# Kernel tuning notes

Hardware: AMD Instinct MI355X
Metric: run time of the kernel (lower is better)

The kernel has to match this reference:

```python
import jax, jax.numpy as jnp
import numpy as np

N, P, C = 100000, 64, 128
DIST_TH = 0.1


def setup_inputs() -> dict:
    key = jax.random.key(0)
    ks = jax.random.split(key, 12)
    xyz = jax.random.uniform(ks[0], (N, 3), jnp.float32) * 10.0  # room coords in [0,10)^3
    feature = jax.random.normal(ks[1], (N, C), jnp.float32)
    center = jax.random.uniform(ks[2], (P, 3), jnp.float32) * 10.0
    normal = jax.random.normal(ks[3], (P, 3), jnp.float32)
    normal = normal / jnp.linalg.norm(normal, axis=1, keepdims=True)
    pmin = center - 1.5  # axis-aligned extent used on axes 0,1
    pmax = center + 1.5
    inp = {
        'feature': feature, 'xyz': xyz,
        'plane_center': center, 'plane_normal': normal,
        'plane_min': pmin, 'plane_max': pmax,
        'W1': jax.random.normal(ks[4], (C, 2 * C), jnp.float32) * (1.0 / np.sqrt(C)),
        's1': jnp.ones((2 * C,), jnp.float32), 'b1': jnp.zeros((2 * C,), jnp.float32),
        'W2': jax.random.normal(ks[5], (2 * C, C), jnp.float32) * (1.0 / np.sqrt(2 * C)),
        's2': jnp.ones((C,), jnp.float32), 'b2': jnp.zeros((C,), jnp.float32),
        'W3': jax.random.normal(ks[6], (C, 1), jnp.float32) * (1.0 / np.sqrt(C)),
        'b3': jnp.zeros((1,), jnp.float32),
        'Wa': jax.random.normal(ks[7], (C, C), jnp.float32) * (1.0 / np.sqrt(C)),
        'Wm': jax.random.normal(ks[8], (C, C), jnp.float32) * (1.0 / np.sqrt(C)),
        'bm': jnp.zeros((C,), jnp.float32),
    }
    return inp


def reference(feature, xyz, plane_center, plane_normal, plane_min, plane_max,
              W1, s1, b1, W2, s2, b2, W3, b3, Wa, Wm, bm):
    # pointwise MLP (shared across planes): fc1 (conv+BN+ReLU), fc2 (conv+BN+ReLU)
    h = jax.nn.relu((feature @ W1) * s1 + b1)          # [N, 2C]
    h2 = jax.nn.relu((h @ W2) * s2 + b2)               # [N, C] == plane_feature
    logit = (h2 @ W3 + b3)[:, 0]                        # [N] fc3 logits (plane_result)

    # per-plane point membership masks (dense [N, P])
    proj = xyz @ plane_normal.T                         # [N, P]
    offs = jnp.sum(plane_center * plane_normal, axis=1) # [P]
    dist_mask = jnp.abs(proj - offs[None, :]) < DIST_TH
    rng = ((xyz[:, None, 0] >= plane_min[None, :, 0]) & (xyz[:, None, 0] < plane_max[None, :, 0]) &
           (xyz[:, None, 1] >= plane_min[None, :, 1]) & (xyz[:, None, 1] < plane_max[None, :, 1]))
    mask = dist_mask & rng                              # [N, P]

    on_sel = jax.nn.sigmoid(logit) > 0.5                # [N]
    on_mask = (mask & on_sel[:, None]).astype(feature.dtype)
    off_mask = (mask & ~on_sel[:, None]).astype(feature.dtype)

    # attention pooling: masked softmax over points, per plane, per channel
    a = h2 @ Wa                                         # [N, C] att activations
    e = jnp.exp(a - jnp.max(a, axis=0, keepdims=True))  # stable exp, [N, C]
    eh = e * h2

    def att_pool(m):                                    # m: [N, P] float
        num = jnp.einsum('np,nc->pc', m, eh)
        den = jnp.einsum('np,nc->pc', m, e)
        agg = num / (den + 1e-9)                        # masked-softmax weighted sum
        return jax.nn.relu(agg @ Wm + bm)               # att_pooling.mlp (conv+ReLU)

    ori = jnp.concatenate([plane_center, plane_normal, plane_min, plane_max], axis=1)  # [P, 12]
    on_feat = jnp.concatenate([att_pool(on_mask), ori], axis=1)    # [P, C+12]
    off_feat = jnp.concatenate([att_pool(off_mask), ori], axis=1)  # [P, C+12]
    return logit, on_feat, off_feat
```

## Files before the change

kernel.cpp:

```cpp
#include <hip/hip_runtime.h>

#define NPTS 100000
#define P 64
#define C 128
#define CHUNKS 16
#define CHUNK_PTS 6250
#define CHUNK_PAD 6400

typedef __bf16 bf16_t;
typedef __bf16 bf16x4 __attribute__((ext_vector_type(4)));
typedef __bf16 bf16x8 __attribute__((ext_vector_type(8)));
typedef float floatx4 __attribute__((ext_vector_type(4)));


__global__ __launch_bounds__(256) void prep_kernel(
    const float* __restrict__ W1, const float* __restrict__ s1,
    const float* __restrict__ W2, const float* __restrict__ s2,
    const float* __restrict__ Wa,
    bf16_t* __restrict__ W1t, bf16_t* __restrict__ W2t, bf16_t* __restrict__ Wat)
{
  int i0 = blockIdx.x * blockDim.x + threadIdx.x;
  int stride = gridDim.x * blockDim.x;
  for (int i = i0; i < 256 * 128; i += stride) {
    int n = i >> 7, k = i & 127;
    W1t[i] = (bf16_t)(W1[k * 256 + n] * s1[n]);
  }
  for (int i = i0; i < 128 * 256; i += stride) {
    int n = i >> 8, k = i & 255;
    W2t[i] = (bf16_t)(W2[k * 128 + n] * s2[n]);
  }
  for (int i = i0; i < 128 * 128; i += stride) {
    int n = i >> 7, k = i & 127;
    Wat[i] = (bf16_t)(Wa[k * 128 + n]);
  }
}

__device__ __forceinline__ void process_tile(
    bf16_t* A1, bf16_t* Hs, bf16_t* aB,
    const float* w3S, const float* b1S, const float* b2S, float b3v,
    const bf16_t* __restrict__ W1t, const bf16_t* __restrict__ W2t,
    const bf16_t* __restrict__ Wat,
    bf16_t* __restrict__ rec, float* __restrict__ out_logit,
    int m0, int tid, int wave, int lane, int quad, int l16)
{
  const floatx4 zero4 = {0.f, 0.f, 0.f, 0.f};

  {
    floatx4 acc[4][4];
#pragma unroll
    for (int mt = 0; mt < 4; ++mt)
#pragma unroll
      for (int nt = 0; nt < 4; ++nt) acc[mt][nt] = zero4;
#pragma unroll
    for (int kt = 0; kt < 4; ++kt) {
      bf16x8 af[4], bf[4];
#pragma unroll
      for (int mt = 0; mt < 4; ++mt)
        af[mt] = *(const bf16x8*)(A1 + (mt * 16 + l16) * 136 + kt * 32 + quad * 8);
#pragma unroll
      for (int nt = 0; nt < 4; ++nt)
        bf[nt] = *(const bf16x8*)(W1t + (wave * 64 + nt * 16 + l16) * 128 + kt * 32 + quad * 8);
#pragma unroll
      for (int mt = 0; mt < 4; ++mt)
#pragma unroll
        for (int nt = 0; nt < 4; ++nt)
          acc[mt][nt] = __builtin_amdgcn_mfma_f32_16x16x32_bf16(af[mt], bf[nt], acc[mt][nt], 0, 0, 0);
    }
#pragma unroll
    for (int nt = 0; nt < 4; ++nt) {
      int col = wave * 64 + nt * 16 + l16;
      float bias = b1S[col];
#pragma unroll
      for (int mt = 0; mt < 4; ++mt)
#pragma unroll
        for (int r = 0; r < 4; ++r) {
          float hv = fmaxf(acc[mt][nt][r] + bias, 0.f);
          Hs[(mt * 16 + quad * 4 + r) * 264 + col] = (bf16_t)hv;
        }
    }
  }
  __syncthreads();

  {
    floatx4 acc[4][2];
#pragma unroll
    for (int mt = 0; mt < 4; ++mt) { acc[mt][0] = zero4; acc[mt][1] = zero4; }
#pragma unroll
    for (int kt = 0; kt < 8; ++kt) {
      bf16x8 af[4], bf[2];
#pragma unroll
      for (int mt = 0; mt < 4; ++mt)
        af[mt] = *(const bf16x8*)(Hs + (mt * 16 + l16) * 264 + kt * 32 + quad * 8);
#pragma unroll
      for (int nt = 0; nt < 2; ++nt)
        bf[nt] = *(const bf16x8*)(W2t + (wave * 32 + nt * 16 + l16) * 256 + kt * 32 + quad * 8);
#pragma unroll
      for (int mt = 0; mt < 4; ++mt)
#pragma unroll
        for (int nt = 0; nt < 2; ++nt)
          acc[mt][nt] = __builtin_amdgcn_mfma_f32_16x16x32_bf16(af[mt], bf[nt], acc[mt][nt], 0, 0, 0);
    }
#pragma unroll
    for (int nt = 0; nt < 2; ++nt) {
      int col = wave * 32 + nt * 16 + l16;
      float bias = b2S[col];
#pragma unroll
      for (int mt = 0; mt < 4; ++mt)
#pragma unroll
        for (int r = 0; r < 4; ++r) {
          float hv = fmaxf(acc[mt][nt][r] + bias, 0.f);
          A1[(mt * 16 + quad * 4 + r) * 136 + col] = (bf16_t)hv;
        }
    }
  }
  __syncthreads();

  {
    floatx4 acc[4][2];
#pragma unroll
    for (int mt = 0; mt < 4; ++mt) { acc[mt][0] = zero4; acc[mt][1] = zero4; }
#pragma unroll
    for (int kt = 0; kt < 4; ++kt) {
      bf16x8 af[4], bf[2];
#pragma unroll
      for (int mt = 0; mt < 4; ++mt)
        af[mt] = *(const bf16x8*)(A1 + (mt * 16 + l16) * 136 + kt * 32 + quad * 8);
#pragma unroll
      for (int nt = 0; nt < 2; ++nt)
        bf[nt] = *(const bf16x8*)(Wat + (wave * 32 + nt * 16 + l16) * 128 + kt * 32 + quad * 8);
#pragma unroll
      for (int mt = 0; mt < 4; ++mt)
#pragma unroll
        for (int nt = 0; nt < 2; ++nt)
          acc[mt][nt] = __builtin_amdgcn_mfma_f32_16x16x32_bf16(af[mt], bf[nt], acc[mt][nt], 0, 0, 0);
    }
#pragma unroll
    for (int nt = 0; nt < 2; ++nt) {
      int col = wave * 32 + nt * 16 + l16;
#pragma unroll
      for (int mt = 0; mt < 4; ++mt)
#pragma unroll
        for (int r = 0; r < 4; ++r)
          aB[(mt * 16 + quad * 4 + r) * 136 + col] = (bf16_t)acc[mt][nt][r];
    }
  }
  __syncthreads();

  {
    const int m = tid >> 2, g = tid & 3, c0g = g * 32;
    const int mg = m0 + m;
    float lsum = 0.f;
#pragma unroll
    for (int cc = 0; cc < 4; ++cc) {
      bf16x8 v = *(const bf16x8*)(A1 + m * 136 + c0g + cc * 8);
#pragma unroll
      for (int j = 0; j < 8; ++j)
        lsum += (float)v[j] * w3S[c0g + cc * 8 + j];
    }
    lsum += __shfl_xor(lsum, 1);
    lsum += __shfl_xor(lsum, 2);
    if (mg < NPTS && g == 0) out_logit[mg] = lsum + b3v;
  }

  for (int i = tid; i < 64 * 64; i += 256) {
    int pt = i >> 6, slot = i & 63;
    if (m0 + pt < NPTS) {
      const bf16_t* src = (slot < 32) ? (aB + pt * 136 + slot * 4)
                                      : (A1 + pt * 136 + (slot - 32) * 4);
      uint2 v = *(const uint2*)src;
      *(uint2*)(rec + (size_t)(m0 + pt) * 256 + slot * 4) = v;
    }
  }
}

__global__ __launch_bounds__(256) void main_kernel(
    const float* __restrict__ feature,
    const float* __restrict__ b1, const float* __restrict__ b2,
    const float* __restrict__ W3, const float* __restrict__ b3,
    const bf16_t* __restrict__ W1t, const bf16_t* __restrict__ W2t,
    const bf16_t* __restrict__ Wat,
    bf16_t* __restrict__ rec, float* __restrict__ out_logit)
{
  __shared__ __align__(16) char smem[17408 + 33792 + 512 + 1024 + 512];
  bf16_t* A1  = (bf16_t*)smem;
  bf16_t* Hs  = (bf16_t*)(smem + 17408);
  bf16_t* aB  = (bf16_t*)(smem + 17408);
  float*  w3S = (float*)(smem + 17408 + 33792);
  float*  b1S = (float*)(smem + 17408 + 33792 + 512);
  float*  b2S = (float*)(smem + 17408 + 33792 + 512 + 1024);

  const int tid  = threadIdx.x;
  const int wave = tid >> 6, lane = tid & 63;
  const int quad = lane >> 4, l16 = lane & 15;
  const int m0 = blockIdx.x * 128;

  if (tid < 128) w3S[tid] = W3[tid];
  if (tid < 128) b2S[tid] = b2[tid];
  b1S[tid] = b1[tid];
  const float b3v = b3[0];

  const int r0 = tid >> 5, c4 = tid & 31;

#pragma unroll
  for (int j = 0; j < 8; ++j) {
    int r = r0 + j * 8;
    float4 v = make_float4(0.f, 0.f, 0.f, 0.f);
    if (m0 + r < NPTS) v = *(const float4*)(feature + (size_t)(m0 + r) * C + c4 * 4);
    bf16x4 o = {(bf16_t)v.x, (bf16_t)v.y, (bf16_t)v.z, (bf16_t)v.w};
    *(bf16x4*)(A1 + r * 136 + c4 * 4) = o;
  }
  __syncthreads();

  float4 f2[8];
#pragma unroll
  for (int j = 0; j < 8; ++j) {
    int r = r0 + j * 8;
    f2[j] = make_float4(0.f, 0.f, 0.f, 0.f);
    if (m0 + 64 + r < NPTS)
      f2[j] = *(const float4*)(feature + (size_t)(m0 + 64 + r) * C + c4 * 4);
  }

  process_tile(A1, Hs, aB, w3S, b1S, b2S, b3v, W1t, W2t, Wat, rec, out_logit,
               m0, tid, wave, lane, quad, l16);
  __syncthreads();

#pragma unroll
  for (int j = 0; j < 8; ++j) {
    int r = r0 + j * 8;
    bf16x4 o = {(bf16_t)f2[j].x, (bf16_t)f2[j].y, (bf16_t)f2[j].z, (bf16_t)f2[j].w};
    *(bf16x4*)(A1 + r * 136 + c4 * 4) = o;
  }
  __syncthreads();

  process_tile(A1, Hs, aB, w3S, b1S, b2S, b3v, W1t, W2t, Wat, rec, out_logit,
               m0 + 64, tid, wave, lane, quad, l16);
}

__global__ __launch_bounds__(256) void pool_kernel(
    const float* __restrict__ xyz, const float* __restrict__ out_logit,
    const bf16_t* __restrict__ rec,
    const float* __restrict__ ctr, const float* __restrict__ nrm,
    const float* __restrict__ pmn, const float* __restrict__ pmx,
    float* __restrict__ partial)
{
  const int plane = blockIdx.x >> 4;
  const int chunk = blockIdx.x & 15;
  const int tid = threadIdx.x, lane = tid & 63;

  __shared__ float accS[4][128];
  for (int i = tid; i < 512; i += 256) ((float*)accS)[i] = 0.f;

  const float nx = nrm[plane * 3], ny = nrm[plane * 3 + 1], nz = nrm[plane * 3 + 2];
  const float offs = ctr[plane * 3] * nx + ctr[plane * 3 + 1] * ny + ctr[plane * 3 + 2] * nz;
  const float mnx = pmn[plane * 3], mny = pmn[plane * 3 + 1];
  const float mxx = pmx[plane * 3], mxy = pmx[plane * 3 + 1];
  __syncthreads();

  const int base = chunk * CHUNK_PTS;
  float nOn0 = 0, nOn1 = 0, dOn0 = 0, dOn1 = 0;
  float nOf0 = 0, nOf1 = 0, dOf0 = 0, dOf1 = 0;

  for (int i = tid; i < CHUNK_PAD; i += 256) {
    int pt = base + i;
    bool hit = false;
    if (i < CHUNK_PTS) {
      float x = xyz[pt * 3], y = xyz[pt * 3 + 1], z = xyz[pt * 3 + 2];
      float proj = x * nx + y * ny + z * nz;
      hit = (fabsf(proj - offs) < 0.1f) &&
            (x >= mnx) && (x < mxx) && (y >= mny) && (y < mxy);
    }
    unsigned long long m = __ballot(hit);
    while (m) {
      int l = __builtin_ctzll(m);
      m &= m - 1;
      int hpt = __shfl(pt, l);
      float lg = out_logit[hpt];
      const unsigned* r32 = (const unsigned*)(rec + (size_t)hpt * 256);
      unsigned ap = r32[lane];
      unsigned hp = r32[64 + lane];
      float a0 = __uint_as_float(ap << 16);
      float a1 = __uint_as_float(ap & 0xffff0000u);
      float h0 = __uint_as_float(hp << 16);
      float h1 = __uint_as_float(hp & 0xffff0000u);
      float e0 = __expf(a0), e1 = __expf(a1);
      if (lg > 0.f) { nOn0 += e0 * h0; nOn1 += e1 * h1; dOn0 += e0; dOn1 += e1; }
      else          { nOf0 += e0 * h0; nOf1 += e1 * h1; dOf0 += e0; dOf1 += e1; }
    }
  }

  atomicAdd(&accS[0][lane * 2],     nOn0);
  atomicAdd(&accS[0][lane * 2 + 1], nOn1);
  atomicAdd(&accS[1][lane * 2],     dOn0);
  atomicAdd(&accS[1][lane * 2 + 1], dOn1);
  atomicAdd(&accS[2][lane * 2],     nOf0);
  atomicAdd(&accS[2][lane * 2 + 1], nOf1);
  atomicAdd(&accS[3][lane * 2],     dOf0);
  atomicAdd(&accS[3][lane * 2 + 1], dOf1);
  __syncthreads();

  float* dst = partial + (size_t)blockIdx.x * 512;
  for (int i = tid; i < 512; i += 256) dst[i] = ((float*)accS)[i];
}

__global__ __launch_bounds__(256) void finalize_kernel(
    const float* __restrict__ partial,
    const float* __restrict__ Wm, const float* __restrict__ bm,
    const float* __restrict__ ctr, const float* __restrict__ nrm,
    const float* __restrict__ pmn, const float* __restrict__ pmx,
    float* __restrict__ out)
{
  int sel = blockIdx.x >> 6, p = blockIdx.x & 63;
  int tid = threadIdx.x, j = tid & 127, half = tid >> 7;
  __shared__ float numS[2][128], denS[2][128], aggS[128], sumS[2][128];

  const float* bp = partial + ((size_t)p * 16 + half * 8) * 512 + sel * 256;
  float num = 0.f, den = 0.f;
#pragma unroll
  for (int k = 0; k < 8; ++k) {
    num += bp[k * 512 + j];
    den += bp[k * 512 + 128 + j];
  }
  numS[half][j] = num;
  denS[half][j] = den;
  __syncthreads();
  if (tid < 128)
    aggS[tid] = (numS[0][tid] + numS[1][tid]) / (denS[0][tid] + denS[1][tid] + 1e-9f);
  __syncthreads();

  float s = 0.f;
  const int cbase = half * 64;
#pragma unroll 8
  for (int c = 0; c < 64; ++c)
    s += aggS[cbase + c] * Wm[(cbase + c) * C + j];
  sumS[half][j] = s;
  __syncthreads();

  float* dst = out + NPTS + sel * (P * 140) + p * 140;
  if (tid < 128)
    dst[tid] = fmaxf(sumS[0][tid] + sumS[1][tid] + bm[tid], 0.f);
  if (tid < 12) {
    float v;
    if (tid < 3)      v = ctr[p * 3 + tid];
    else if (tid < 6) v = nrm[p * 3 + tid - 3];
    else if (tid < 9) v = pmn[p * 3 + tid - 6];
    else              v = pmx[p * 3 + tid - 9];
    dst[C + tid] = v;
  }
}

extern "C" void kernel_launch(void* const* d_in, const int* in_sizes, int n_in,
                              void* d_out, int out_size, void* d_ws, size_t ws_size,
                              hipStream_t stream)
{
  const float* feature = (const float*)d_in[0];
  const float* xyz     = (const float*)d_in[1];
  const float* ctr     = (const float*)d_in[2];
  const float* nrm     = (const float*)d_in[3];
  const float* pmn     = (const float*)d_in[4];
  const float* pmx     = (const float*)d_in[5];
  const float* W1      = (const float*)d_in[6];
  const float* s1      = (const float*)d_in[7];
  const float* b1      = (const float*)d_in[8];
  const float* W2      = (const float*)d_in[9];
  const float* s2      = (const float*)d_in[10];
  const float* b2      = (const float*)d_in[11];
  const float* W3      = (const float*)d_in[12];
  const float* b3      = (const float*)d_in[13];
  const float* Wa      = (const float*)d_in[14];
  const float* Wm      = (const float*)d_in[15];
  const float* bm      = (const float*)d_in[16];
  float* out = (float*)d_out;

  char* ws = (char*)d_ws;
  bf16_t* W1t = (bf16_t*)(ws);
  bf16_t* W2t = (bf16_t*)(ws + 65536);
  bf16_t* Wat = (bf16_t*)(ws + 131072);
  bf16_t* rec = (bf16_t*)(ws + 163840);
  float* partial = (float*)(ws + 163840 + (size_t)NPTS * 512);

  prep_kernel<<<64, 256, 0, stream>>>(W1, s1, W2, s2, Wa, W1t, W2t, Wat);
  main_kernel<<<(NPTS + 127) / 128, 256, 0, stream>>>(
      feature, b1, b2, W3, b3, W1t, W2t, Wat, rec, out);
  pool_kernel<<<64 * CHUNKS, 256, 0, stream>>>(
      xyz, out, rec, ctr, nrm, pmn, pmx, partial);
  finalize_kernel<<<128, 256, 0, stream>>>(partial, Wm, bm, ctr, nrm, pmn, pmx, out);
}
```

Before: 196.9 us.

## Shrink MLP kernel tile to 32 points per block for higher occupancy

```diff
diff --git a/kernel.cpp b/kernel.cpp
--- a/kernel.cpp
+++ b/kernel.cpp
@@ -35,145 +35,7 @@
   }
 }
 
-__device__ __forceinline__ void process_tile(
-    bf16_t* A1, bf16_t* Hs, bf16_t* aB,
-    const float* w3S, const float* b1S, const float* b2S, float b3v,
-    const bf16_t* __restrict__ W1t, const bf16_t* __restrict__ W2t,
-    const bf16_t* __restrict__ Wat,
-    bf16_t* __restrict__ rec, float* __restrict__ out_logit,
-    int m0, int tid, int wave, int lane, int quad, int l16)
-{
-  const floatx4 zero4 = {0.f, 0.f, 0.f, 0.f};
-
-  {
-    floatx4 acc[4][4];
-#pragma unroll
-    for (int mt = 0; mt < 4; ++mt)
-#pragma unroll
-      for (int nt = 0; nt < 4; ++nt) acc[mt][nt] = zero4;
-#pragma unroll
-    for (int kt = 0; kt < 4; ++kt) {
-      bf16x8 af[4], bf[4];
-#pragma unroll
-      for (int mt = 0; mt < 4; ++mt)
-        af[mt] = *(const bf16x8*)(A1 + (mt * 16 + l16) * 136 + kt * 32 + quad * 8);
-#pragma unroll
-      for (int nt = 0; nt < 4; ++nt)
-        bf[nt] = *(const bf16x8*)(W1t + (wave * 64 + nt * 16 + l16) * 128 + kt * 32 + quad * 8);
-#pragma unroll
-      for (int mt = 0; mt < 4; ++mt)
-#pragma unroll
-        for (int nt = 0; nt < 4; ++nt)
-          acc[mt][nt] = __builtin_amdgcn_mfma_f32_16x16x32_bf16(af[mt], bf[nt], acc[mt][nt], 0, 0, 0);
-    }
-#pragma unroll
-    for (int nt = 0; nt < 4; ++nt) {
-      int col = wave * 64 + nt * 16 + l16;
-      float bias = b1S[col];
-#pragma unroll
-      for (int mt = 0; mt < 4; ++mt)
-#pragma unroll
-        for (int r = 0; r < 4; ++r) {
-          float hv = fmaxf(acc[mt][nt][r] + bias, 0.f);
-          Hs[(mt * 16 + quad * 4 + r) * 264 + col] = (bf16_t)hv;
-        }
-    }
-  }
-  __syncthreads();
-
-  {
-    floatx4 acc[4][2];
-#pragma unroll
-    for (int mt = 0; mt < 4; ++mt) { acc[mt][0] = zero4; acc[mt][1] = zero4; }
-#pragma unroll
-    for (int kt = 0; kt < 8; ++kt) {
-      bf16x8 af[4], bf[2];
-#pragma unroll
-      for (int mt = 0; mt < 4; ++mt)
-        af[mt] = *(const bf16x8*)(Hs + (mt * 16 + l16) * 264 + kt * 32 + quad * 8);
-#pragma unroll
-      for (int nt = 0; nt < 2; ++nt)
-        bf[nt] = *(const bf16x8*)(W2t + (wave * 32 + nt * 16 + l16) * 256 + kt * 32 + quad * 8);
-#pragma unroll
-      for (int mt = 0; mt < 4; ++mt)
-#pragma unroll
-        for (int nt = 0; nt < 2; ++nt)
-          acc[mt][nt] = __builtin_amdgcn_mfma_f32_16x16x32_bf16(af[mt], bf[nt], acc[mt][nt], 0, 0, 0);
-    }
-#pragma unroll
-    for (int nt = 0; nt < 2; ++nt) {
-      int col = wave * 32 + nt * 16 + l16;
-      float bias = b2S[col];
-#pragma unroll
-      for (int mt = 0; mt < 4; ++mt)
-#pragma unroll
-        for (int r = 0; r < 4; ++r) {
-          float hv = fmaxf(acc[mt][nt][r] + bias, 0.f);
-          A1[(mt * 16 + quad * 4 + r) * 136 + col] = (bf16_t)hv;
-        }
-    }
-  }
-  __syncthreads();
-
-  {
-    floatx4 acc[4][2];
-#pragma unroll
-    for (int mt = 0; mt < 4; ++mt) { acc[mt][0] = zero4; acc[mt][1] = zero4; }
-#pragma unroll
-    for (int kt = 0; kt < 4; ++kt) {
-      bf16x8 af[4], bf[2];
-#pragma unroll
-      for (int mt = 0; mt < 4; ++mt)
-        af[mt] = *(const bf16x8*)(A1 + (mt * 16 + l16) * 136 + kt * 32 + quad * 8);
-#pragma unroll
-      for (int nt = 0; nt < 2; ++nt)
-        bf[nt] = *(const bf16x8*)(Wat + (wave * 32 + nt * 16 + l16) * 128 + kt * 32 + quad * 8);
-#pragma unroll
-      for (int mt = 0; mt < 4; ++mt)
-#pragma unroll
-        for (int nt = 0; nt < 2; ++nt)
-          acc[mt][nt] = __builtin_amdgcn_mfma_f32_16x16x32_bf16(af[mt], bf[nt], acc[mt][nt], 0, 0, 0);
-    }
-#pragma unroll
-    for (int nt = 0; nt < 2; ++nt) {
-      int col = wave * 32 + nt * 16 + l16;
-#pragma unroll
-      for (int mt = 0; mt < 4; ++mt)
-#pragma unroll
-        for (int r = 0; r < 4; ++r)
-          aB[(mt * 16 + quad * 4 + r) * 136 + col] = (bf16_t)acc[mt][nt][r];
-    }
-  }
-  __syncthreads();
-
-  {
-    const int m = tid >> 2, g = tid & 3, c0g = g * 32;
-    const int mg = m0 + m;
-    float lsum = 0.f;
-#pragma unroll
-    for (int cc = 0; cc < 4; ++cc) {
-      bf16x8 v = *(const bf16x8*)(A1 + m * 136 + c0g + cc * 8);
-#pragma unroll
-      for (int j = 0; j < 8; ++j)
-        lsum += (float)v[j] * w3S[c0g + cc * 8 + j];
-    }
-    lsum += __shfl_xor(lsum, 1);
-    lsum += __shfl_xor(lsum, 2);
-    if (mg < NPTS && g == 0) out_logit[mg] = lsum + b3v;
-  }
-
-  for (int i = tid; i < 64 * 64; i += 256) {
-    int pt = i >> 6, slot = i & 63;
-    if (m0 + pt < NPTS) {
-      const bf16_t* src = (slot < 32) ? (aB + pt * 136 + slot * 4)
-                                      : (A1 + pt * 136 + (slot - 32) * 4);
-      uint2 v = *(const uint2*)src;
-      *(uint2*)(rec + (size_t)(m0 + pt) * 256 + slot * 4) = v;
-    }
-  }
-}
-
-__global__ __launch_bounds__(256) void main_kernel(
+__global__ __launch_bounds__(256, 6) void main_kernel(
     const float* __restrict__ feature,
     const float* __restrict__ b1, const float* __restrict__ b2,
     const float* __restrict__ W3, const float* __restrict__ b3,
@@ -181,59 +43,156 @@
     const bf16_t* __restrict__ Wat,
     bf16_t* __restrict__ rec, float* __restrict__ out_logit)
 {
-  __shared__ __align__(16) char smem[17408 + 33792 + 512 + 1024 + 512];
+  __shared__ __align__(16) char smem[8704 + 16896 + 512];
   bf16_t* A1  = (bf16_t*)smem;
-  bf16_t* Hs  = (bf16_t*)(smem + 17408);
-  bf16_t* aB  = (bf16_t*)(smem + 17408);
-  float*  w3S = (float*)(smem + 17408 + 33792);
-  float*  b1S = (float*)(smem + 17408 + 33792 + 512);
-  float*  b2S = (float*)(smem + 17408 + 33792 + 512 + 1024);
+  bf16_t* Hs  = (bf16_t*)(smem + 8704);
+  bf16_t* aB  = (bf16_t*)(smem + 8704);
+  float*  w3S = (float*)(smem + 8704 + 16896);
 
   const int tid  = threadIdx.x;
   const int wave = tid >> 6, lane = tid & 63;
   const int quad = lane >> 4, l16 = lane & 15;
-  const int m0 = blockIdx.x * 128;
+  const int m0 = blockIdx.x * 32;
 
   if (tid < 128) w3S[tid] = W3[tid];
-  if (tid < 128) b2S[tid] = b2[tid];
-  b1S[tid] = b1[tid];
-  const float b3v = b3[0];
-
-  const int r0 = tid >> 5, c4 = tid & 31;
-
-#pragma unroll
-  for (int j = 0; j < 8; ++j) {
-    int r = r0 + j * 8;
-    float4 v = make_float4(0.f, 0.f, 0.f, 0.f);
-    if (m0 + r < NPTS) v = *(const float4*)(feature + (size_t)(m0 + r) * C + c4 * 4);
+
+#pragma unroll
+  for (int j = 0; j < 4; ++j) {
+    int idx = j * 256 + tid;
+    int r = idx >> 5, c4 = idx & 31;
+    float4 v = *(const float4*)(feature + (size_t)(m0 + r) * C + c4 * 4);
     bf16x4 o = {(bf16_t)v.x, (bf16_t)v.y, (bf16_t)v.z, (bf16_t)v.w};
     *(bf16x4*)(A1 + r * 136 + c4 * 4) = o;
   }
   __syncthreads();
 
-  float4 f2[8];
-#pragma unroll
-  for (int j = 0; j < 8; ++j) {
-    int r = r0 + j * 8;
-    f2[j] = make_float4(0.f, 0.f, 0.f, 0.f);
-    if (m0 + 64 + r < NPTS)
-      f2[j] = *(const float4*)(feature + (size_t)(m0 + 64 + r) * C + c4 * 4);
-  }
-
-  process_tile(A1, Hs, aB, w3S, b1S, b2S, b3v, W1t, W2t, Wat, rec, out_logit,
-               m0, tid, wave, lane, quad, l16);
-  __syncthreads();
-
-#pragma unroll
-  for (int j = 0; j < 8; ++j) {
-    int r = r0 + j * 8;
-    bf16x4 o = {(bf16_t)f2[j].x, (bf16_t)f2[j].y, (bf16_t)f2[j].z, (bf16_t)f2[j].w};
-    *(bf16x4*)(A1 + r * 136 + c4 * 4) = o;
-  }
-  __syncthreads();
-
-  process_tile(A1, Hs, aB, w3S, b1S, b2S, b3v, W1t, W2t, Wat, rec, out_logit,
-               m0 + 64, tid, wave, lane, quad, l16);
+  const floatx4 zero4 = {0.f, 0.f, 0.f, 0.f};
+
+  {
+    floatx4 acc[2][4];
+#pragma unroll
+    for (int mt = 0; mt < 2; ++mt)
+#pragma unroll
+      for (int nt = 0; nt < 4; ++nt) acc[mt][nt] = zero4;
+#pragma unroll
+    for (int kt = 0; kt < 4; ++kt) {
+      bf16x8 af[2], bf[4];
+#pragma unroll
+      for (int mt = 0; mt < 2; ++mt)
+        af[mt] = *(const bf16x8*)(A1 + (mt * 16 + l16) * 136 + kt * 32 + quad * 8);
+#pragma unroll
+      for (int nt = 0; nt < 4; ++nt)
+        bf[nt] = *(const bf16x8*)(W1t + (wave * 64 + nt * 16 + l16) * 128 + kt * 32 + quad * 8);
+#pragma unroll
+      for (int mt = 0; mt < 2; ++mt)
+#pragma unroll
+        for (int nt = 0; nt < 4; ++nt)
+          acc[mt][nt] = __builtin_amdgcn_mfma_f32_16x16x32_bf16(af[mt], bf[nt], acc[mt][nt], 0, 0, 0);
+    }
+#pragma unroll
+    for (int nt = 0; nt < 4; ++nt) {
+      int col = wave * 64 + nt * 16 + l16;
+      float bias = b1[col];
+#pragma unroll
+      for (int mt = 0; mt < 2; ++mt)
+#pragma unroll
+        for (int r = 0; r < 4; ++r) {
+          float hv = fmaxf(acc[mt][nt][r] + bias, 0.f);
+          Hs[(mt * 16 + quad * 4 + r) * 264 + col] = (bf16_t)hv;
+        }
+    }
+  }
+  __syncthreads();
+
+  {
+    floatx4 acc[2][2];
+#pragma unroll
+    for (int mt = 0; mt < 2; ++mt) { acc[mt][0] = zero4; acc[mt][1] = zero4; }
+#pragma unroll
+    for (int kt = 0; kt < 8; ++kt) {
+      bf16x8 af[2], bf[2];
+#pragma unroll
+      for (int mt = 0; mt < 2; ++mt)
+        af[mt] = *(const bf16x8*)(Hs + (mt * 16 + l16) * 264 + kt * 32 + quad * 8);
+#pragma unroll
+      for (int nt = 0; nt < 2; ++nt)
+        bf[nt] = *(const bf16x8*)(W2t + (wave * 32 + nt * 16 + l16) * 256 + kt * 32 + quad * 8);
+#pragma unroll
+      for (int mt = 0; mt < 2; ++mt)
+#pragma unroll
+        for (int nt = 0; nt < 2; ++nt)
+          acc[mt][nt] = __builtin_amdgcn_mfma_f32_16x16x32_bf16(af[mt], bf[nt], acc[mt][nt], 0, 0, 0);
+    }
+#pragma unroll
+    for (int nt = 0; nt < 2; ++nt) {
+      int col = wave * 32 + nt * 16 + l16;
+      float bias = b2[col];
+#pragma unroll
+      for (int mt = 0; mt < 2; ++mt)
+#pragma unroll
+        for (int r = 0; r < 4; ++r) {
+          float hv = fmaxf(acc[mt][nt][r] + bias, 0.f);
+          A1[(mt * 16 + quad * 4 + r) * 136 + col] = (bf16_t)hv;
+        }
+    }
+  }
+  __syncthreads();
+
+  {
+    floatx4 acc[2][2];
+#pragma unroll
+    for (int mt = 0; mt < 2; ++mt) { acc[mt][0] = zero4; acc[mt][1] = zero4; }
+#pragma unroll
+    for (int kt = 0; kt < 4; ++kt) {
+      bf16x8 af[2], bf[2];
+#pragma unroll
+      for (int mt = 0; mt < 2; ++mt)
+        af[mt] = *(const bf16x8*)(A1 + (mt * 16 + l16) * 136 + kt * 32 + quad * 8);
+#pragma unroll
+      for (int nt = 0; nt < 2; ++nt)
+        bf[nt] = *(const bf16x8*)(Wat + (wave * 32 + nt * 16 + l16) * 128 + kt * 32 + quad * 8);
+#pragma unroll
+      for (int mt = 0; mt < 2; ++mt)
+#pragma unroll
+        for (int nt = 0; nt < 2; ++nt)
+          acc[mt][nt] = __builtin_amdgcn_mfma_f32_16x16x32_bf16(af[mt], bf[nt], acc[mt][nt], 0, 0, 0);
+    }
+#pragma unroll
+    for (int nt = 0; nt < 2; ++nt) {
+      int col = wave * 32 + nt * 16 + l16;
+#pragma unroll
+      for (int mt = 0; mt < 2; ++mt)
+#pragma unroll
+        for (int r = 0; r < 4; ++r)
+          aB[(mt * 16 + quad * 4 + r) * 136 + col] = (bf16_t)acc[mt][nt][r];
+    }
+  }
+  __syncthreads();
+
+  {
+    const int m = tid >> 3, g = tid & 7, c0g = g * 16;
+    float lsum = 0.f;
+#pragma unroll
+    for (int cc = 0; cc < 2; ++cc) {
+      bf16x8 v = *(const bf16x8*)(A1 + m * 136 + c0g + cc * 8);
+#pragma unroll
+      for (int j = 0; j < 8; ++j)
+        lsum += (float)v[j] * w3S[c0g + cc * 8 + j];
+    }
+    lsum += __shfl_xor(lsum, 1);
+    lsum += __shfl_xor(lsum, 2);
+    lsum += __shfl_xor(lsum, 4);
+    if (g == 0) out_logit[m0 + m] = lsum + b3[0];
+  }
+
+#pragma unroll
+  for (int i = tid; i < 32 * 64; i += 256) {
+    int pt = i >> 6, slot = i & 63;
+    const bf16_t* src = (slot < 32) ? (aB + pt * 136 + slot * 4)
+                                    : (A1 + pt * 136 + (slot - 32) * 4);
+    uint2 v = *(const uint2*)src;
+    *(uint2*)(rec + (size_t)(m0 + pt) * 256 + slot * 4) = v;
+  }
 }
 
 __global__ __launch_bounds__(256) void pool_kernel(
@@ -379,7 +338,7 @@
   float* partial = (float*)(ws + 163840 + (size_t)NPTS * 512);
 
   prep_kernel<<<64, 256, 0, stream>>>(W1, s1, W2, s2, Wa, W1t, W2t, Wat);
-  main_kernel<<<(NPTS + 127) / 128, 256, 0, stream>>>(
+  main_kernel<<<NPTS / 32, 256, 0, stream>>>(
       feature, b1, b2, W3, b3, W1t, W2t, Wat, rec, out);
   pool_kernel<<<64 * CHUNKS, 256, 0, stream>>>(
       xyz, out, rec, ctr, nrm, pmn, pmx, partial);
```

Result: slower. 204.1 us (+3.6%).

## Hold MLP weight fragments in registers and process one 64-point tile per block

Applied to the files above, without the earlier changes.

```diff
diff --git a/kernel.cpp b/kernel.cpp
--- a/kernel.cpp
+++ b/kernel.cpp
@@ -7,6 +7,9 @@
 #define CHUNK_PTS 6250
 #define CHUNK_PAD 6400
 
+#define SA 138
+#define SH 266
+
 typedef __bf16 bf16_t;
 typedef __bf16 bf16x4 __attribute__((ext_vector_type(4)));
 typedef __bf16 bf16x8 __attribute__((ext_vector_type(8)));
@@ -35,145 +38,7 @@
   }
 }
 
-__device__ __forceinline__ void process_tile(
-    bf16_t* A1, bf16_t* Hs, bf16_t* aB,
-    const float* w3S, const float* b1S, const float* b2S, float b3v,
-    const bf16_t* __restrict__ W1t, const bf16_t* __restrict__ W2t,
-    const bf16_t* __restrict__ Wat,
-    bf16_t* __restrict__ rec, float* __restrict__ out_logit,
-    int m0, int tid, int wave, int lane, int quad, int l16)
-{
-  const floatx4 zero4 = {0.f, 0.f, 0.f, 0.f};
-
-  {
-    floatx4 acc[4][4];
-#pragma unroll
-    for (int mt = 0; mt < 4; ++mt)
-#pragma unroll
-      for (int nt = 0; nt < 4; ++nt) acc[mt][nt] = zero4;
-#pragma unroll
-    for (int kt = 0; kt < 4; ++kt) {
-      bf16x8 af[4], bf[4];
-#pragma unroll
-      for (int mt = 0; mt < 4; ++mt)
-        af[mt] = *(const bf16x8*)(A1 + (mt * 16 + l16) * 136 + kt * 32 + quad * 8);
-#pragma unroll
-      for (int nt = 0; nt < 4; ++nt)
-        bf[nt] = *(const bf16x8*)(W1t + (wave * 64 + nt * 16 + l16) * 128 + kt * 32 + quad * 8);
-#pragma unroll
-      for (int mt = 0; mt < 4; ++mt)
-#pragma unroll
-        for (int nt = 0; nt < 4; ++nt)
-          acc[mt][nt] = __builtin_amdgcn_mfma_f32_16x16x32_bf16(af[mt], bf[nt], acc[mt][nt], 0, 0, 0);
-    }
-#pragma unroll
-    for (int nt = 0; nt < 4; ++nt) {
-      int col = wave * 64 + nt * 16 + l16;
-      float bias = b1S[col];
-#pragma unroll
-      for (int mt = 0; mt < 4; ++mt)
-#pragma unroll
-        for (int r = 0; r < 4; ++r) {
-          float hv = fmaxf(acc[mt][nt][r] + bias, 0.f);
-          Hs[(mt * 16 + quad * 4 + r) * 264 + col] = (bf16_t)hv;
-        }
-    }
-  }
-  __syncthreads();
-
-  {
-    floatx4 acc[4][2];
-#pragma unroll
-    for (int mt = 0; mt < 4; ++mt) { acc[mt][0] = zero4; acc[mt][1] = zero4; }
-#pragma unroll
-    for (int kt = 0; kt < 8; ++kt) {
-      bf16x8 af[4], bf[2];
-#pragma unroll
-      for (int mt = 0; mt < 4; ++mt)
-        af[mt] = *(const bf16x8*)(Hs + (mt * 16 + l16) * 264 + kt * 32 + quad * 8);
-#pragma unroll
-      for (int nt = 0; nt < 2; ++nt)
-        bf[nt] = *(const bf16x8*)(W2t + (wave * 32 + nt * 16 + l16) * 256 + kt * 32 + quad * 8);
-#pragma unroll
-      for (int mt = 0; mt < 4; ++mt)
-#pragma unroll
-        for (int nt = 0; nt < 2; ++nt)
-          acc[mt][nt] = __builtin_amdgcn_mfma_f32_16x16x32_bf16(af[mt], bf[nt], acc[mt][nt], 0, 0, 0);
-    }
-#pragma unroll
-    for (int nt = 0; nt < 2; ++nt) {
-      int col = wave * 32 + nt * 16 + l16;
-      float bias = b2S[col];
-#pragma unroll
-      for (int mt = 0; mt < 4; ++mt)
-#pragma unroll
-        for (int r = 0; r < 4; ++r) {
-          float hv = fmaxf(acc[mt][nt][r] + bias, 0.f);
-          A1[(mt * 16 + quad * 4 + r) * 136 + col] = (bf16_t)hv;
-        }
-    }
-  }
-  __syncthreads();
-
-  {
-    floatx4 acc[4][2];
-#pragma unroll
-    for (int mt = 0; mt < 4; ++mt) { acc[mt][0] = zero4; acc[mt][1] = zero4; }
-#pragma unroll
-    for (int kt = 0; kt < 4; ++kt) {
-      bf16x8 af[4], bf[2];
-#pragma unroll
-      for (int mt = 0; mt < 4; ++mt)
-        af[mt] = *(const bf16x8*)(A1 + (mt * 16 + l16) * 136 + kt * 32 + quad * 8);
-#pragma unroll
-      for (int nt = 0; nt < 2; ++nt)
-        bf[nt] = *(const bf16x8*)(Wat + (wave * 32 + nt * 16 + l16) * 128 + kt * 32 + quad * 8);
-#pragma unroll
-      for (int mt = 0; mt < 4; ++mt)
-#pragma unroll
-        for (int nt = 0; nt < 2; ++nt)
-          acc[mt][nt] = __builtin_amdgcn_mfma_f32_16x16x32_bf16(af[mt], bf[nt], acc[mt][nt], 0, 0, 0);
-    }
-#pragma unroll
-    for (int nt = 0; nt < 2; ++nt) {
-      int col = wave * 32 + nt * 16 + l16;
-#pragma unroll
-      for (int mt = 0; mt < 4; ++mt)
-#pragma unroll
-        for (int r = 0; r < 4; ++r)
-          aB[(mt * 16 + quad * 4 + r) * 136 + col] = (bf16_t)acc[mt][nt][r];
-    }
-  }
-  __syncthreads();
-
-  {
-    const int m = tid >> 2, g = tid & 3, c0g = g * 32;
-    const int mg = m0 + m;
-    float lsum = 0.f;
-#pragma unroll
-    for (int cc = 0; cc < 4; ++cc) {
-      bf16x8 v = *(const bf16x8*)(A1 + m * 136 + c0g + cc * 8);
-#pragma unroll
-      for (int j = 0; j < 8; ++j)
-        lsum += (float)v[j] * w3S[c0g + cc * 8 + j];
-    }
-    lsum += __shfl_xor(lsum, 1);
-    lsum += __shfl_xor(lsum, 2);
-    if (mg < NPTS && g == 0) out_logit[mg] = lsum + b3v;
-  }
-
-  for (int i = tid; i < 64 * 64; i += 256) {
-    int pt = i >> 6, slot = i & 63;
-    if (m0 + pt < NPTS) {
-      const bf16_t* src = (slot < 32) ? (aB + pt * 136 + slot * 4)
-                                      : (A1 + pt * 136 + (slot - 32) * 4);
-      uint2 v = *(const uint2*)src;
-      *(uint2*)(rec + (size_t)(m0 + pt) * 256 + slot * 4) = v;
-    }
-  }
-}
-
-__global__ __launch_bounds__(256) void main_kernel(
+__global__ __launch_bounds__(256, 2) void main_kernel(
     const float* __restrict__ feature,
     const float* __restrict__ b1, const float* __restrict__ b2,
     const float* __restrict__ W3, const float* __restrict__ b3,
@@ -181,59 +46,168 @@
     const bf16_t* __restrict__ Wat,
     bf16_t* __restrict__ rec, float* __restrict__ out_logit)
 {
-  __shared__ __align__(16) char smem[17408 + 33792 + 512 + 1024 + 512];
+  __shared__ __align__(16) char smem[17664 + 34048 + 512];
   bf16_t* A1  = (bf16_t*)smem;
-  bf16_t* Hs  = (bf16_t*)(smem + 17408);
-  bf16_t* aB  = (bf16_t*)(smem + 17408);
-  float*  w3S = (float*)(smem + 17408 + 33792);
-  float*  b1S = (float*)(smem + 17408 + 33792 + 512);
-  float*  b2S = (float*)(smem + 17408 + 33792 + 512 + 1024);
+  bf16_t* Hs  = (bf16_t*)(smem + 17664);
+  bf16_t* aB  = (bf16_t*)(smem + 17664);
+  float*  w3S = (float*)(smem + 17664 + 34048);
 
   const int tid  = threadIdx.x;
   const int wave = tid >> 6, lane = tid & 63;
   const int quad = lane >> 4, l16 = lane & 15;
-  const int m0 = blockIdx.x * 128;
+  const int m0 = blockIdx.x * 64;
 
   if (tid < 128) w3S[tid] = W3[tid];
-  if (tid < 128) b2S[tid] = b2[tid];
-  b1S[tid] = b1[tid];
-  const float b3v = b3[0];
-
-  const int r0 = tid >> 5, c4 = tid & 31;
-
-#pragma unroll
-  for (int j = 0; j < 8; ++j) {
-    int r = r0 + j * 8;
-    float4 v = make_float4(0.f, 0.f, 0.f, 0.f);
-    if (m0 + r < NPTS) v = *(const float4*)(feature + (size_t)(m0 + r) * C + c4 * 4);
-    bf16x4 o = {(bf16_t)v.x, (bf16_t)v.y, (bf16_t)v.z, (bf16_t)v.w};
-    *(bf16x4*)(A1 + r * 136 + c4 * 4) = o;
-  }
-  __syncthreads();
-
-  float4 f2[8];
-#pragma unroll
-  for (int j = 0; j < 8; ++j) {
-    int r = r0 + j * 8;
-    f2[j] = make_float4(0.f, 0.f, 0.f, 0.f);
-    if (m0 + 64 + r < NPTS)
-      f2[j] = *(const float4*)(feature + (size_t)(m0 + 64 + r) * C + c4 * 4);
-  }
-
-  process_tile(A1, Hs, aB, w3S, b1S, b2S, b3v, W1t, W2t, Wat, rec, out_logit,
-               m0, tid, wave, lane, quad, l16);
-  __syncthreads();
-
-#pragma unroll
-  for (int j = 0; j < 8; ++j) {
-    int r = r0 + j * 8;
-    bf16x4 o = {(bf16_t)f2[j].x, (bf16_t)f2[j].y, (bf16_t)f2[j].z, (bf16_t)f2[j].w};
-    *(bf16x4*)(A1 + r * 136 + c4 * 4) = o;
-  }
-  __syncthreads();
-
-  process_tile(A1, Hs, aB, w3S, b1S, b2S, b3v, W1t, W2t, Wat, rec, out_logit,
-               m0 + 64, tid, wave, lane, quad, l16);
+
+  bf16x8 w1f[4][4], w2f[8][2], waf[4][2];
+#pragma unroll
+  for (int kt = 0; kt < 4; ++kt)
+#pragma unroll
+    for (int nt = 0; nt < 4; ++nt)
+      w1f[kt][nt] = *(const bf16x8*)(W1t + (wave * 64 + nt * 16 + l16) * 128 + kt * 32 + quad * 8);
+#pragma unroll
+  for (int kt = 0; kt < 8; ++kt)
+#pragma unroll
+    for (int nt = 0; nt < 2; ++nt)
+      w2f[kt][nt] = *(const bf16x8*)(W2t + (wave * 32 + nt * 16 + l16) * 256 + kt * 32 + quad * 8);
+#pragma unroll
+  for (int kt = 0; kt < 4; ++kt)
+#pragma unroll
+    for (int nt = 0; nt < 2; ++nt)
+      waf[kt][nt] = *(const bf16x8*)(Wat + (wave * 32 + nt * 16 + l16) * 128 + kt * 32 + quad * 8);
+
+  {
+    const int r0 = tid >> 5, c4 = tid & 31;
+#pragma unroll
+    for (int j = 0; j < 8; ++j) {
+      int r = r0 + j * 8;
+      float4 v = make_float4(0.f, 0.f, 0.f, 0.f);
+      if (m0 + r < NPTS) v = *(const float4*)(feature + (size_t)(m0 + r) * C + c4 * 4);
+      bf16x4 o = {(bf16_t)v.x, (bf16_t)v.y, (bf16_t)v.z, (bf16_t)v.w};
+      *(bf16x4*)(A1 + r * SA + c4 * 4) = o;
+    }
+  }
+  __syncthreads();
+
+  const floatx4 zero4 = {0.f, 0.f, 0.f, 0.f};
+
+  {
+    floatx4 acc[4][4];
+#pragma unroll
+    for (int mt = 0; mt < 4; ++mt)
+#pragma unroll
+      for (int nt = 0; nt < 4; ++nt) acc[mt][nt] = zero4;
+#pragma unroll
+    for (int kt = 0; kt < 4; ++kt) {
+      bf16x8 af[4];
+#pragma unroll
+      for (int mt = 0; mt < 4; ++mt)
+        af[mt] = *(const bf16x8*)(A1 + (mt * 16 + l16) * SA + kt * 32 + quad * 8);
+#pragma unroll
+      for (int mt = 0; mt < 4; ++mt)
+#pragma unroll
+        for (int nt = 0; nt < 4; ++nt)
+          acc[mt][nt] = __builtin_amdgcn_mfma_f32_16x16x32_bf16(af[mt], w1f[kt][nt], acc[mt][nt], 0, 0, 0);
+    }
+#pragma unroll
+    for (int nt = 0; nt < 4; ++nt) {
+      int col = wave * 64 + nt * 16 + l16;
+      float bias = b1[col];
+#pragma unroll
+      for (int mt = 0; mt < 4; ++mt)
+#pragma unroll
+        for (int r = 0; r < 4; ++r) {
+          float hv = fmaxf(acc[mt][nt][r] + bias, 0.f);
+          Hs[(mt * 16 + quad * 4 + r) * SH + col] = (bf16_t)hv;
+        }
+    }
+  }
+  __syncthreads();
+
+  {
+    floatx4 acc[4][2];
+#pragma unroll
+    for (int mt = 0; mt < 4; ++mt) { acc[mt][0] = zero4; acc[mt][1] = zero4; }
+#pragma unroll
+    for (int kt = 0; kt < 8; ++kt) {
+      bf16x8 af[4];
+#pragma unroll
+      for (int mt = 0; mt < 4; ++mt)
+        af[mt] = *(const bf16x8*)(Hs + (mt * 16 + l16) * SH + kt * 32 + quad * 8);
+#pragma unroll
+      for (int mt = 0; mt < 4; ++mt)
+#pragma unroll
+        for (int nt = 0; nt < 2; ++nt)
+          acc[mt][nt] = __builtin_amdgcn_mfma_f32_16x16x32_bf16(af[mt], w2f[kt][nt], acc[mt][nt], 0, 0, 0);
+    }
+#pragma unroll
+    for (int nt = 0; nt < 2; ++nt) {
+      int col = wave * 32 + nt * 16 + l16;
+      float bias = b2[col];
+#pragma unroll
+      for (int mt = 0; mt < 4; ++mt)
+#pragma unroll
+        for (int r = 0; r < 4; ++r) {
+          float hv = fmaxf(acc[mt][nt][r] + bias, 0.f);
+          A1[(mt * 16 + quad * 4 + r) * SA + col] = (bf16_t)hv;
+        }
+    }
+  }
+  __syncthreads();
+
+  {
+    floatx4 acc[4][2];
+#pragma unroll
+    for (int mt = 0; mt < 4; ++mt) { acc[mt][0] = zero4; acc[mt][1] = zero4; }
+#pragma unroll
+    for (int kt = 0; kt < 4; ++kt) {
+      bf16x8 af[4];
+#pragma unroll
+      for (int mt = 0; mt < 4; ++mt)
+        af[mt] = *(const bf16x8*)(A1 + (mt * 16 + l16) * SA + kt * 32 + quad * 8);
+#pragma unroll
+      for (int mt = 0; mt < 4; ++mt)
+#pragma unroll
+        for (int nt = 0; nt < 2; ++nt)
+          acc[mt][nt] = __builtin_amdgcn_mfma_f32_16x16x32_bf16(af[mt], waf[kt][nt], acc[mt][nt], 0, 0, 0);
+    }
+#pragma unroll
+    for (int nt = 0; nt < 2; ++nt) {
+      int col = wave * 32 + nt * 16 + l16;
+#pragma unroll
+      for (int mt = 0; mt < 4; ++mt)
+#pragma unroll
+        for (int r = 0; r < 4; ++r)
+          aB[(mt * 16 + quad * 4 + r) * SA + col] = (bf16_t)acc[mt][nt][r];
+    }
+  }
+  __syncthreads();
+
+  {
+    const int m = tid >> 2, g = tid & 3, c0g = g * 32;
+    const int mg = m0 + m;
+    float lsum = 0.f;
+#pragma unroll
+    for (int cc = 0; cc < 4; ++cc) {
+      bf16x8 v = *(const bf16x8*)(A1 + m * SA + c0g + cc * 8);
+#pragma unroll
+      for (int j = 0; j < 8; ++j)
+        lsum += (float)v[j] * w3S[c0g + cc * 8 + j];
+    }
+    lsum += __shfl_xor(lsum, 1);
+    lsum += __shfl_xor(lsum, 2);
+    if (mg < NPTS && g == 0) out_logit[mg] = lsum + b3[0];
+  }
+
+  for (int i = tid; i < 64 * 64; i += 256) {
+    int pt = i >> 6, slot = i & 63;
+    if (m0 + pt < NPTS) {
+      const bf16_t* src = (slot < 32) ? (aB + pt * SA + slot * 4)
+                                      : (A1 + pt * SA + (slot - 32) * 4);
+      uint2 v = *(const uint2*)src;
+      *(uint2*)(rec + (size_t)(m0 + pt) * 256 + slot * 4) = v;
+    }
+  }
 }
 
 __global__ __launch_bounds__(256) void pool_kernel(
@@ -379,7 +353,7 @@
   float* partial = (float*)(ws + 163840 + (size_t)NPTS * 512);
 
   prep_kernel<<<64, 256, 0, stream>>>(W1, s1, W2, s2, Wa, W1t, W2t, Wat);
-  main_kernel<<<(NPTS + 127) / 128, 256, 0, stream>>>(
+  main_kernel<<<(NPTS + 63) / 64, 256, 0, stream>>>(
       feature, b1, b2, W3, b3, W1t, W2t, Wat, rec, out);
   pool_kernel<<<64 * CHUNKS, 256, 0, stream>>>(
       xyz, out, rec, ctr, nrm, pmn, pmx, partial);
```

New measurement: 243.1 us. 1.23x slower.

## Compute plane masks in MLP kernel and compact hit points for pooling

Applied to the files above, without the earlier changes.

```diff
diff --git a/kernel.cpp b/kernel.cpp
--- a/kernel.cpp
+++ b/kernel.cpp
@@ -3,9 +3,7 @@
 #define NPTS 100000
 #define P 64
 #define C 128
-#define CHUNKS 16
-#define CHUNK_PTS 6250
-#define CHUNK_PAD 6400
+#define CAP 50000
 
 typedef __bf16 bf16_t;
 typedef __bf16 bf16x4 __attribute__((ext_vector_type(4)));
@@ -35,14 +33,59 @@
   }
 }
 
-__device__ __forceinline__ void process_tile(
-    bf16_t* A1, bf16_t* Hs, bf16_t* aB,
-    const float* w3S, const float* b1S, const float* b2S, float b3v,
+__global__ __launch_bounds__(256) void main_kernel(
+    const float* __restrict__ feature, const float* __restrict__ xyz,
+    const float* __restrict__ ctr, const float* __restrict__ nrm,
+    const float* __restrict__ pmn, const float* __restrict__ pmx,
+    const float* __restrict__ b1, const float* __restrict__ b2,
+    const float* __restrict__ W3, const float* __restrict__ b3,
     const bf16_t* __restrict__ W1t, const bf16_t* __restrict__ W2t,
     const bf16_t* __restrict__ Wat,
-    bf16_t* __restrict__ rec, float* __restrict__ out_logit,
-    int m0, int tid, int wave, int lane, int quad, int l16)
+    unsigned* __restrict__ gctr, unsigned long long* __restrict__ masksG,
+    float* __restrict__ logitG, bf16_t* __restrict__ ahG,
+    float* __restrict__ out_logit)
 {
+  __shared__ __align__(16) char smem[17408 + 33792 + 2048 + 512];
+  bf16_t* A1  = (bf16_t*)smem;
+  bf16_t* Hs  = (bf16_t*)(smem + 17408);
+  bf16_t* aB  = (bf16_t*)(smem + 17408);
+  unsigned long long* maskS = (unsigned long long*)(smem + 34816);
+  float*    logitS = (float*)(smem + 35328);
+  unsigned* idxS   = (unsigned*)(smem + 35584);
+  unsigned* ctrlS  = (unsigned*)(smem + 35840);
+  float*    plS    = (float*)(smem + 51200);
+  float*    w3S    = (float*)(smem + 53248);
+
+  const int tid  = threadIdx.x;
+  const int wave = tid >> 6, lane = tid & 63;
+  const int quad = lane >> 4, l16 = lane & 15;
+  const int m0 = blockIdx.x * 64;
+  const int m = tid >> 2, g = tid & 3;
+  const int mg = m0 + m;
+
+  if (tid < 128) w3S[tid] = W3[tid];
+  if (tid < 64) {
+    int p = tid;
+    float nx = nrm[p * 3 + 0], ny = nrm[p * 3 + 1], nz = nrm[p * 3 + 2];
+    float cx = ctr[p * 3 + 0], cy = ctr[p * 3 + 1], cz = ctr[p * 3 + 2];
+    plS[p * 8 + 0] = nx; plS[p * 8 + 1] = ny; plS[p * 8 + 2] = nz;
+    plS[p * 8 + 3] = cx * nx + cy * ny + cz * nz;
+    plS[p * 8 + 4] = pmn[p * 3 + 0]; plS[p * 8 + 5] = pmn[p * 3 + 1];
+    plS[p * 8 + 6] = pmx[p * 3 + 0]; plS[p * 8 + 7] = pmx[p * 3 + 1];
+  }
+
+  float px = -1e9f, py = -1e9f, pz = -1e9f;
+  if (mg < NPTS) { px = xyz[mg * 3]; py = xyz[mg * 3 + 1]; pz = xyz[mg * 3 + 2]; }
+
+  for (int i = tid; i < 64 * 32; i += 256) {
+    int r = i >> 5, c4 = i & 31;
+    float4 v = make_float4(0.f, 0.f, 0.f, 0.f);
+    if (m0 + r < NPTS) v = *(const float4*)(feature + (size_t)(m0 + r) * C + c4 * 4);
+    bf16_t* dst = A1 + r * 136 + c4 * 4;
+    dst[0] = (bf16_t)v.x; dst[1] = (bf16_t)v.y; dst[2] = (bf16_t)v.z; dst[3] = (bf16_t)v.w;
+  }
+  __syncthreads();
+
   const floatx4 zero4 = {0.f, 0.f, 0.f, 0.f};
 
   {
@@ -69,7 +112,7 @@
 #pragma unroll
     for (int nt = 0; nt < 4; ++nt) {
       int col = wave * 64 + nt * 16 + l16;
-      float bias = b1S[col];
+      float bias = b1[col];
 #pragma unroll
       for (int mt = 0; mt < 4; ++mt)
 #pragma unroll
@@ -103,7 +146,7 @@
 #pragma unroll
     for (int nt = 0; nt < 2; ++nt) {
       int col = wave * 32 + nt * 16 + l16;
-      float bias = b2S[col];
+      float bias = b2[col];
 #pragma unroll
       for (int mt = 0; mt < 4; ++mt)
 #pragma unroll
@@ -147,9 +190,8 @@
   __syncthreads();
 
   {
-    const int m = tid >> 2, g = tid & 3, c0g = g * 32;
-    const int mg = m0 + m;
     float lsum = 0.f;
+    const int c0g = g * 32;
 #pragma unroll
     for (int cc = 0; cc < 4; ++cc) {
       bf16x8 v = *(const bf16x8*)(A1 + m * 136 + c0g + cc * 8);
@@ -159,88 +201,68 @@
     }
     lsum += __shfl_xor(lsum, 1);
     lsum += __shfl_xor(lsum, 2);
-    if (mg < NPTS && g == 0) out_logit[mg] = lsum + b3v;
-  }
-
-  for (int i = tid; i < 64 * 64; i += 256) {
-    int pt = i >> 6, slot = i & 63;
-    if (m0 + pt < NPTS) {
-      const bf16_t* src = (slot < 32) ? (aB + pt * 136 + slot * 4)
-                                      : (A1 + pt * 136 + (slot - 32) * 4);
-      uint2 v = *(const uint2*)src;
-      *(uint2*)(rec + (size_t)(m0 + pt) * 256 + slot * 4) = v;
+    float logit = lsum + b3[0];
+    if (mg < NPTS && g == 0) { out_logit[mg] = logit; logitS[m] = logit; }
+  }
+
+  {
+    unsigned bits = 0;
+#pragma unroll 4
+    for (int k = 0; k < 16; ++k) {
+      const float* pl = plS + (g * 16 + k) * 8;
+      float proj = px * pl[0] + py * pl[1] + pz * pl[2];
+      bool h = (fabsf(proj - pl[3]) < 0.1f) &&
+               (px >= pl[4]) && (px < pl[6]) && (py >= pl[5]) && (py < pl[7]);
+      bits |= (h ? 1u : 0u) << k;
+    }
+    unsigned long long msk = ((unsigned long long)bits) << (g * 16);
+    msk |= __shfl_xor(msk, 1);
+    msk |= __shfl_xor(msk, 2);
+    if (g == 0) maskS[m] = msk;
+  }
+  __syncthreads();
+
+  if (tid < 64) {
+    unsigned long long mm = maskS[tid];
+    unsigned long long bal = __ballot(mm != 0ull);
+    if (tid == 0) {
+      unsigned c = (unsigned)__popcll(bal);
+      unsigned b = 0;
+      if (c) b = atomicAdd(gctr, c);
+      ctrlS[0] = b; ctrlS[1] = c;
+    }
+    unsigned r = (unsigned)__popcll(bal & ((1ull << tid) - 1ull));
+    if (mm != 0ull) idxS[r] = (unsigned)tid;
+  }
+  __syncthreads();
+
+  {
+    const unsigned base = ctrlS[0], cnt = ctrlS[1];
+    for (unsigned i = tid; i < cnt * 64; i += 256) {
+      unsigned j = i >> 6, slot = i & 63;
+      unsigned dj = base + j;
+      if (dj < CAP) {
+        int pt = (int)idxS[j];
+        const bf16_t* src = (slot < 32) ? (aB + pt * 136 + slot * 4)
+                                        : (A1 + pt * 136 + (slot - 32) * 4);
+        uint2 v = *(const uint2*)src;
+        *(uint2*)(ahG + (size_t)dj * 256 + slot * 4) = v;
+      }
+    }
+    for (unsigned i = tid; i < cnt; i += 256) {
+      unsigned dj = base + i;
+      if (dj < CAP) {
+        int pt = (int)idxS[i];
+        masksG[dj] = maskS[pt];
+        logitG[dj] = logitS[pt];
+      }
     }
   }
 }
 
-__global__ __launch_bounds__(256) void main_kernel(
-    const float* __restrict__ feature,
-    const float* __restrict__ b1, const float* __restrict__ b2,
-    const float* __restrict__ W3, const float* __restrict__ b3,
-    const bf16_t* __restrict__ W1t, const bf16_t* __restrict__ W2t,
-    const bf16_t* __restrict__ Wat,
-    bf16_t* __restrict__ rec, float* __restrict__ out_logit)
-{
-  __shared__ __align__(16) char smem[17408 + 33792 + 512 + 1024 + 512];
-  bf16_t* A1  = (bf16_t*)smem;
-  bf16_t* Hs  = (bf16_t*)(smem + 17408);
-  bf16_t* aB  = (bf16_t*)(smem + 17408);
-  float*  w3S = (float*)(smem + 17408 + 33792);
-  float*  b1S = (float*)(smem + 17408 + 33792 + 512);
-  float*  b2S = (float*)(smem + 17408 + 33792 + 512 + 1024);
-
-  const int tid  = threadIdx.x;
-  const int wave = tid >> 6, lane = tid & 63;
-  const int quad = lane >> 4, l16 = lane & 15;
-  const int m0 = blockIdx.x * 128;
-
-  if (tid < 128) w3S[tid] = W3[tid];
-  if (tid < 128) b2S[tid] = b2[tid];
-  b1S[tid] = b1[tid];
-  const float b3v = b3[0];
-
-  const int r0 = tid >> 5, c4 = tid & 31;
-
-#pragma unroll
-  for (int j = 0; j < 8; ++j) {
-    int r = r0 + j * 8;
-    float4 v = make_float4(0.f, 0.f, 0.f, 0.f);
-    if (m0 + r < NPTS) v = *(const float4*)(feature + (size_t)(m0 + r) * C + c4 * 4);
-    bf16x4 o = {(bf16_t)v.x, (bf16_t)v.y, (bf16_t)v.z, (bf16_t)v.w};
-    *(bf16x4*)(A1 + r * 136 + c4 * 4) = o;
-  }
-  __syncthreads();
-
-  float4 f2[8];
-#pragma unroll
-  for (int j = 0; j < 8; ++j) {
-    int r = r0 + j * 8;
-    f2[j] = make_float4(0.f, 0.f, 0.f, 0.f);
-    if (m0 + 64 + r < NPTS)
-      f2[j] = *(const float4*)(feature + (size_t)(m0 + 64 + r) * C + c4 * 4);
-  }
-
-  process_tile(A1, Hs, aB, w3S, b1S, b2S, b3v, W1t, W2t, Wat, rec, out_logit,
-               m0, tid, wave, lane, quad, l16);
-  __syncthreads();
-
-#pragma unroll
-  for (int j = 0; j < 8; ++j) {
-    int r = r0 + j * 8;
-    bf16x4 o = {(bf16_t)f2[j].x, (bf16_t)f2[j].y, (bf16_t)f2[j].z, (bf16_t)f2[j].w};
-    *(bf16x4*)(A1 + r * 136 + c4 * 4) = o;
-  }
-  __syncthreads();
-
-  process_tile(A1, Hs, aB, w3S, b1S, b2S, b3v, W1t, W2t, Wat, rec, out_logit,
-               m0 + 64, tid, wave, lane, quad, l16);
-}
-
 __global__ __launch_bounds__(256) void pool_kernel(
-    const float* __restrict__ xyz, const float* __restrict__ out_logit,
-    const bf16_t* __restrict__ rec,
-    const float* __restrict__ ctr, const float* __restrict__ nrm,
-    const float* __restrict__ pmn, const float* __restrict__ pmx,
+    const unsigned long long* __restrict__ masksG, const float* __restrict__ logitG,
+    const bf16_t* __restrict__ ahG, const unsigned* __restrict__ gctr,
     float* __restrict__ partial)
 {
   const int plane = blockIdx.x >> 4;
@@ -249,33 +271,25 @@
 
   __shared__ float accS[4][128];
   for (int i = tid; i < 512; i += 256) ((float*)accS)[i] = 0.f;
-
-  const float nx = nrm[plane * 3], ny = nrm[plane * 3 + 1], nz = nrm[plane * 3 + 2];
-  const float offs = ctr[plane * 3] * nx + ctr[plane * 3 + 1] * ny + ctr[plane * 3 + 2] * nz;
-  const float mnx = pmn[plane * 3], mny = pmn[plane * 3 + 1];
-  const float mxx = pmx[plane * 3], mxy = pmx[plane * 3 + 1];
-  __syncthreads();
-
-  const int base = chunk * CHUNK_PTS;
+  __syncthreads();
+
+  unsigned M = gctr[0]; if (M > CAP) M = CAP;
+  const unsigned j0 = (unsigned)(((unsigned long long)chunk * M) / 16);
+  const unsigned j1 = (unsigned)(((unsigned long long)(chunk + 1) * M) / 16);
+
   float nOn0 = 0, nOn1 = 0, dOn0 = 0, dOn1 = 0;
   float nOf0 = 0, nOf1 = 0, dOf0 = 0, dOf1 = 0;
 
-  for (int i = tid; i < CHUNK_PAD; i += 256) {
-    int pt = base + i;
-    bool hit = false;
-    if (i < CHUNK_PTS) {
-      float x = xyz[pt * 3], y = xyz[pt * 3 + 1], z = xyz[pt * 3 + 2];
-      float proj = x * nx + y * ny + z * nz;
-      hit = (fabsf(proj - offs) < 0.1f) &&
-            (x >= mnx) && (x < mxx) && (y >= mny) && (y < mxy);
-    }
+  for (unsigned jb = j0; jb < j1; jb += 256) {
+    unsigned j = jb + tid;
+    bool hit = (j < j1) && ((masksG[j] >> plane) & 1ull);
     unsigned long long m = __ballot(hit);
     while (m) {
       int l = __builtin_ctzll(m);
       m &= m - 1;
-      int hpt = __shfl(pt, l);
-      float lg = out_logit[hpt];
-      const unsigned* r32 = (const unsigned*)(rec + (size_t)hpt * 256);
+      unsigned jj = __shfl(j, l);
+      float lg = logitG[jj];
+      const unsigned* r32 = (const unsigned*)(ahG) + (size_t)jj * 128;
       unsigned ap = r32[lane];
       unsigned hp = r32[64 + lane];
       float a0 = __uint_as_float(ap << 16);
@@ -375,13 +389,17 @@
   bf16_t* W1t = (bf16_t*)(ws);
   bf16_t* W2t = (bf16_t*)(ws + 65536);
   bf16_t* Wat = (bf16_t*)(ws + 131072);
-  bf16_t* rec = (bf16_t*)(ws + 163840);
-  float* partial = (float*)(ws + 163840 + (size_t)NPTS * 512);
-
+  unsigned* gctr = (unsigned*)(ws + 163840);
+  unsigned long long* masksG = (unsigned long long*)(ws + 163904);
+  float* logitG = (float*)(ws + 563904);
+  bf16_t* ahG = (bf16_t*)(ws + 763904);
+  float* partial = (float*)(ws + 763904 + (size_t)CAP * 512);
+
+  hipMemsetAsync(gctr, 0, 4, stream);
   prep_kernel<<<64, 256, 0, stream>>>(W1, s1, W2, s2, Wa, W1t, W2t, Wat);
-  main_kernel<<<(NPTS + 127) / 128, 256, 0, stream>>>(
-      feature, b1, b2, W3, b3, W1t, W2t, Wat, rec, out);
-  pool_kernel<<<64 * CHUNKS, 256, 0, stream>>>(
-      xyz, out, rec, ctr, nrm, pmn, pmx, partial);
+  main_kernel<<<(NPTS + 63) / 64, 256, 0, stream>>>(
+      feature, xyz, ctr, nrm, pmn, pmx, b1, b2, W3, b3, W1t, W2t, Wat,
+      gctr, masksG, logitG, ahG, out);
+  pool_kernel<<<64 * 16, 256, 0, stream>>>(masksG, logitG, ahG, gctr, partial);
   finalize_kernel<<<128, 256, 0, stream>>>(partial, Wm, bm, ctr, nrm, pmn, pmx, out);
 }
```

Measured after the change: 199.2 us. No clear change (+1.2%).
